# Optimization experiments

Measured on AMD Instinct MI355X. Metric: run time of the kernel, lower is better.

## Reference

```python
import jax, jax.numpy as jnp
import numpy as np

SEQ = 512; WIN = [4, 4, 4]; INNER = 5; DM = 256; H = 4; DK = 64; NEG = -1e9

def _all_sizes():
    s = [SEQ]
    for w in WIN:
        s.append(s[-1] // w)
    return s

def _build_mask():
    # Pyraformer get_mask: intra-scale band (inner_size) + inter-scale parent/child links.
    sizes = _all_sizes(); N = sum(sizes)
    starts = np.cumsum([0] + sizes)
    allow = np.zeros((N, N), bool)
    iw = INNER // 2
    for li, sz in enumerate(sizes):
        st = int(starts[li])
        for i in range(st, st + sz):
            allow[i, max(i - iw, st):min(i + iw + 1, st + sz)] = True
    for li in range(1, len(sizes)):
        st = int(starts[li])
        for i in range(st, st + sizes[li]):
            ls = int(starts[li - 1]) + (i - st) * WIN[li - 1]
            rs = st if i == st + sizes[li] - 1 else int(starts[li - 1]) + (i - st + 1) * WIN[li - 1]
            allow[i, ls:rs] = True
            allow[ls:rs, i] = True
    return jnp.asarray(~allow)  # True = blocked

def _build_indexes():
    # Pyraformer refer_points: for each base position, index of its node at every scale.
    sizes = _all_sizes(); starts = np.cumsum([0] + sizes)
    idx = np.zeros((SEQ, len(sizes)), np.int32)
    for i in range(SEQ):
        cur = i
        idx[i, 0] = cur
        for j in range(1, len(sizes)):
            inner = cur - int(starts[j - 1])
            cur = int(starts[j]) + min(inner // WIN[j - 1], sizes[j] - 1)
            idx[i, j] = cur
    return jnp.asarray(idx)

def _pos_enc(L, D):
    pos = np.arange(L)[:, None]
    div = np.exp(np.arange(0, D, 2) * (-np.log(10000.0) / D))
    pe = np.zeros((L, D), np.float32)
    pe[:, 0::2] = np.sin(pos * div)
    pe[:, 1::2] = np.cos(pos * div)
    return jnp.asarray(pe)

MASK = _build_mask()
INDEXES = _build_indexes()
PE = _pos_enc(SEQ, DM)
DN = ('NCH', 'OIH', 'NCH')

def _ln(x, g, b, eps=1e-5):
    m = x.mean(-1, keepdims=True)
    v = ((x - m) ** 2).mean(-1, keepdims=True)
    return (x - m) * jax.lax.rsqrt(v + eps) * g + b

def _forward(x_enc, x_mark, W_val, W_time, b_time, W_down, b_down, W_conv, b_conv, bn_g, bn_b, W_up, b_up, ln_c_g, ln_c_b, Wq, bq, Wk, bk, Wv, bv, Wo, bo, ln1_g, ln1_b, W1f, b1f, W2f, b2f, ln2_g, ln2_b, Wp, bp):
    B = x_enc.shape[0]
    # DataEmbedding: circular k=3 token conv + time-feature linear + fixed positional
    xt = jnp.pad(x_enc.transpose(0, 2, 1), ((0, 0), (0, 0), (1, 1)), mode='wrap')
    val = jax.lax.conv_general_dilated(xt, W_val, (1,), 'VALID', dimension_numbers=DN).transpose(0, 2, 1)
    emb = val + x_mark @ W_time + b_time + PE[None]  # [B, SEQ, DM]
    # CSCM Bottleneck_Construct: down-proj, strided conv pooling per scale, up-proj, concat, LN
    t = (emb @ W_down + b_down).transpose(0, 2, 1)  # [B, 64, SEQ]
    pooled = []
    for i in range(len(WIN)):
        t = jax.lax.conv_general_dilated(t, W_conv[i], (WIN[i],), 'VALID', dimension_numbers=DN) + b_conv[i][None, :, None]
        t = jax.nn.elu(t * bn_g[i][None, :, None] + bn_b[i][None, :, None])
        pooled.append(t)
    pooled = jnp.concatenate(pooled, axis=2).transpose(0, 2, 1) @ W_up + b_up  # [B, 168, DM]
    x = _ln(jnp.concatenate([emb, pooled], axis=1), ln_c_g, ln_c_b)  # [B, 680, DM]
    N = x.shape[1]
    scale = np.float32(1.0 / np.sqrt(DK))
    for l in range(Wq.shape[0]):
        q = (x @ Wq[l] + bq[l]).reshape(B, N, H, DK).transpose(0, 2, 1, 3)
        k = (x @ Wk[l] + bk[l]).reshape(B, N, H, DK).transpose(0, 2, 1, 3)
        v = (x @ Wv[l] + bv[l]).reshape(B, N, H, DK).transpose(0, 2, 1, 3)
        s = jnp.einsum('bhqd,bhkd->bhqk', q, k) * scale
        s = jnp.where(MASK[None, None], NEG, s)
        o = jnp.einsum('bhqk,bhkd->bhqd', jax.nn.softmax(s, axis=-1), v)
        o = o.transpose(0, 2, 1, 3).reshape(B, N, DM) @ Wo[l] + bo[l]
        x = _ln(x + o, ln1_g[l], ln1_b[l])  # post-norm (normalize_before=False)
        f = jax.nn.relu(x @ W1f[l] + b1f[l]) @ W2f[l] + b2f[l]
        x = _ln(x + f, ln2_g[l], ln2_b[l])
    # FC decoder path: gather each position's multi-scale nodes, concat features
    gathered = x[:, INDEXES.reshape(-1)].reshape(B, SEQ, -1)  # [B, SEQ, 4*DM]
    return gathered[:, -1] @ Wp + bp  # [B, 96]

def setup_inputs() -> dict:
    key = jax.random.key(0)
    ks = iter(jax.random.split(key, 64))
    def w(shape, s=0.05):
        return jax.random.normal(next(ks), shape, jnp.float32) * s
    d = {}
    d['x_enc'] = jax.random.normal(next(ks), (32, SEQ, 1), jnp.float32)
    d['x_mark'] = jax.random.normal(next(ks), (32, SEQ, 4), jnp.float32)
    d['W_val'] = w((DM, 1, 3))
    d['W_time'] = w((4, DM)); d['b_time'] = jnp.zeros((DM,), jnp.float32)
    d['W_down'] = w((DM, 64)); d['b_down'] = jnp.zeros((64,), jnp.float32)
    d['W_conv'] = w((3, 64, 64, 4)); d['b_conv'] = jnp.zeros((3, 64), jnp.float32)
    d['bn_g'] = jnp.ones((3, 64), jnp.float32); d['bn_b'] = jnp.zeros((3, 64), jnp.float32)
    d['W_up'] = w((64, DM)); d['b_up'] = jnp.zeros((DM,), jnp.float32)
    d['ln_c_g'] = jnp.ones((DM,), jnp.float32); d['ln_c_b'] = jnp.zeros((DM,), jnp.float32)
    d['Wq'] = w((2, DM, DM)); d['bq'] = jnp.zeros((2, DM), jnp.float32)
    d['Wk'] = w((2, DM, DM)); d['bk'] = jnp.zeros((2, DM), jnp.float32)
    d['Wv'] = w((2, DM, DM)); d['bv'] = jnp.zeros((2, DM), jnp.float32)
    d['Wo'] = w((2, DM, DM)); d['bo'] = jnp.zeros((2, DM), jnp.float32)
    d['ln1_g'] = jnp.ones((2, DM), jnp.float32); d['ln1_b'] = jnp.zeros((2, DM), jnp.float32)
    d['W1f'] = w((2, DM, 512)); d['b1f'] = jnp.zeros((2, 512), jnp.float32)
    d['W2f'] = w((2, 512, DM)); d['b2f'] = jnp.zeros((2, DM), jnp.float32)
    d['ln2_g'] = jnp.ones((2, DM), jnp.float32); d['ln2_b'] = jnp.zeros((2, DM), jnp.float32)
    d['Wp'] = w((4 * DM, 96)); d['bp'] = jnp.zeros((96,), jnp.float32)
    return d

def reference(x_enc, x_mark, W_val, W_time, b_time, W_down, b_down, W_conv, b_conv, bn_g, bn_b, W_up, b_up, ln_c_g, ln_c_b, Wq, bq, Wk, bk, Wv, bv, Wo, bo, ln1_g, ln1_b, W1f, b1f, W2f, b2f, ln2_g, ln2_b, Wp, bp):
    return _forward(x_enc, x_mark, W_val, W_time, b_time, W_down, b_down, W_conv, b_conv, bn_g, bn_b, W_up, b_up, ln_c_g, ln_c_b, Wq, bq, Wk, bk, Wv, bv, Wo, bo, ln1_g, ln1_b, W1f, b1f, W2f, b2f, ln2_g, ln2_b, Wp, bp)
```

## Files before the change

### kernel.cpp

```cpp
#include <hip/hip_runtime.h>
#include <hip/hip_bf16.h>
#include <math.h>

#define B 32
#define SEQ 512
#define NTOK 680
#define DM 256
#define FF 512
#define NROWS (B*NTOK)

using bf16x8 = __attribute__((ext_vector_type(8))) short;
using f32x4  = __attribute__((ext_vector_type(4))) float;
using u32x4  = __attribute__((ext_vector_type(4))) unsigned int;
typedef __hip_bfloat16 bf16;

__device__ __forceinline__ unsigned short f2bf(float f) {
    union { float f; unsigned u; } x; x.f = f;
    unsigned r = (x.u + 0x7fffu + ((x.u >> 16) & 1u)) >> 16;
    return (unsigned short)r;
}
__device__ __forceinline__ float bfu2f(unsigned short u) {
    union { unsigned u; float f; } x; x.u = ((unsigned)u) << 16;
    return x.f;
}
__device__ __forceinline__ void dotu(unsigned a, unsigned b, float& s) {
    union { unsigned u; float f; } al, ah, bl, bh;
    al.u = a << 16; ah.u = a & 0xffff0000u;
    bl.u = b << 16; bh.u = b & 0xffff0000u;
    s = fmaf(al.f, bl.f, s);
    s = fmaf(ah.f, bh.f, s);
}

__global__ __launch_bounds__(256) void emb_kernel(
    const float* __restrict__ x_enc, const float* __restrict__ x_mark,
    const float* __restrict__ W_val, const float* __restrict__ W_time,
    const float* __restrict__ b_time, float* __restrict__ X, bf16* __restrict__ Xe)
{
    int bs = blockIdx.x;
    int b = bs >> 9, s = bs & 511;
    int d = threadIdx.x;
    int sm1 = (s + 511) & 511, sp1 = (s + 1) & 511;
    float x0 = x_enc[b*512 + sm1];
    float x1 = x_enc[b*512 + s];
    float x2 = x_enc[b*512 + sp1];
    float val = x0 * W_val[d*3+0] + x1 * W_val[d*3+1] + x2 * W_val[d*3+2];
    const float* mk = &x_mark[(size_t)bs*4];
    float tm = mk[0]*W_time[d] + mk[1]*W_time[256+d] + mk[2]*W_time[512+d] + mk[3]*W_time[768+d];
    int i2 = d & ~1;
    float div = expf((float)i2 * (-9.210340371976184f / 256.0f));
    float ang = (float)s * div;
    float pe = (d & 1) ? cosf(ang) : sinf(ang);
    float out = val + tm + b_time[d] + pe;
    X[((size_t)(b*NTOK + s))*DM + d] = out;
    ((unsigned short*)Xe)[(size_t)bs*DM + d] = f2bf(out);
}

__global__ __launch_bounds__(64) void conv_kernel(
    const float* __restrict__ in, int inRPB, int inOff,
    float* __restrict__ Pool, int outOff, int Lout,
    const float* __restrict__ W_conv, const float* __restrict__ b_conv,
    const float* __restrict__ bn_g, const float* __restrict__ bn_b, int sc)
{
    __shared__ float lds[256];
    int blk = blockIdx.x;
    int b = blk / Lout, p = blk % Lout;
    int t = threadIdx.x;
    for (int u = t; u < 256; u += 64)
        lds[u] = in[((size_t)(b*inRPB + inOff + p*4 + (u >> 6)))*64 + (u & 63)];
    __syncthreads();
    float acc = b_conv[sc*64 + t];
    const float* w = &W_conv[(size_t)(sc*64 + t)*256];
    #pragma unroll 4
    for (int ci = 0; ci < 64; ++ci) {
        #pragma unroll
        for (int tap = 0; tap < 4; ++tap)
            acc = fmaf(lds[tap*64 + ci], w[ci*4 + tap], acc);
    }
    float v = acc * bn_g[sc*64 + t] + bn_b[sc*64 + t];
    v = v > 0.f ? v : expm1f(v);
    Pool[((size_t)(b*168 + outOff + p))*64 + t] = v;
}

__global__ __launch_bounds__(256) void up_kernel(
    const float* __restrict__ Pool, const float* __restrict__ W_up,
    const float* __restrict__ b_up, float* __restrict__ X)
{
    __shared__ float row[64];
    int blk = blockIdx.x;
    int b = blk / 168, p = blk % 168;
    int d = threadIdx.x;
    if (d < 64) row[d] = Pool[(size_t)blk*64 + d];
    __syncthreads();
    float acc = b_up[d];
    #pragma unroll 8
    for (int k = 0; k < 64; ++k) acc = fmaf(row[k], W_up[k*256 + d], acc);
    X[((size_t)(b*NTOK + 512 + p))*DM + d] = acc;
}

__global__ __launch_bounds__(256) void ln_kernel(
    const float* __restrict__ Xf, bf16* __restrict__ Xio,
    const float* __restrict__ g, const float* __restrict__ bta)
{
    int r = blockIdx.x*4 + (threadIdx.x >> 6);
    int lane = threadIdx.x & 63;
    float4 v = ((const float4*)(Xf + (size_t)r*DM))[lane];
    float s = v.x + v.y + v.z + v.w;
    #pragma unroll
    for (int o = 32; o; o >>= 1) s += __shfl_xor(s, o);
    float mean = s * (1.0f/256.0f);
    float dx = v.x-mean, dy = v.y-mean, dz = v.z-mean, dw = v.w-mean;
    float q = dx*dx + dy*dy + dz*dz + dw*dw;
    #pragma unroll
    for (int o = 32; o; o >>= 1) q += __shfl_xor(q, o);
    float inv = rsqrtf(q*(1.0f/256.0f) + 1e-5f);
    float4 gg = ((const float4*)g)[lane];
    float4 bb = ((const float4*)bta)[lane];
    float ox = dx*inv*gg.x + bb.x;
    float oy = dy*inv*gg.y + bb.y;
    float oz = dz*inv*gg.z + bb.z;
    float ow = dw*inv*gg.w + bb.w;
    unsigned u0 = (unsigned)f2bf(ox) | ((unsigned)f2bf(oy) << 16);
    unsigned u1 = (unsigned)f2bf(oz) | ((unsigned)f2bf(ow) << 16);
    ((uint2*)(Xio + (size_t)r*DM))[lane] = make_uint2(u0, u1);
}

__global__ void nbr_kernel(int* __restrict__ nbr, int* __restrict__ ncnt)
{
    int i = blockIdx.x * 64 + threadIdx.x;
    if (i >= NTOK) return;
    const int starts[5] = {0, 512, 640, 672, 680};
    int si = (i < 512) ? 0 : (i < 640) ? 1 : (i < 672) ? 2 : 3;
    int st = starts[si], en = starts[si+1];
    int idx = i - st;
    int cnt = 0;
    if (si >= 1) {
        int cs = starts[si-1] + idx*4;
        #pragma unroll
        for (int c = 0; c < 4; ++c) nbr[i*16 + cnt++] = cs + c;
    }
    int lo = (i-2 > st) ? i-2 : st;
    int hi = (i+2 < en-1) ? i+2 : en-1;
    for (int j = lo; j <= hi; ++j) nbr[i*16 + cnt++] = j;
    if (si <= 2) nbr[i*16 + cnt++] = starts[si+1] + (idx >> 2);
    ncnt[i] = cnt;
}

__global__ __launch_bounds__(256) void attn_kernel(
    const bf16* __restrict__ Q, const bf16* __restrict__ K,
    const bf16* __restrict__ V, bf16* __restrict__ O,
    const int* __restrict__ nbr, const int* __restrict__ ncnt)
{
    __shared__ float wsm[4][16];
    __shared__ int   jsm[4][16];
    int flat = blockIdx.x;
    int row = (flat & 7) * (NROWS/8) + (flat >> 3);
    int n = row % NTOK, b = row / NTOK;
    int h = threadIdx.x >> 6;
    int lane = threadIdx.x & 63;
    int j = lane >> 2, g = lane & 3;
    int cnt = ncnt[n];
    int nj = (j < cnt) ? nbr[n*16 + j] : n;
    int jr = b*NTOK + nj;

    const uint4* qp = (const uint4*)(Q + (size_t)row*DM + h*64 + g*16);
    const uint4* kp = (const uint4*)(K + (size_t)jr*DM + h*64 + g*16);
    uint4 qa = qp[0], qb = qp[1];
    uint4 ka = kp[0], kb = kp[1];
    float s = 0.f;
    dotu(qa.x, ka.x, s); dotu(qa.y, ka.y, s); dotu(qa.z, ka.z, s); dotu(qa.w, ka.w, s);
    dotu(qb.x, kb.x, s); dotu(qb.y, kb.y, s); dotu(qb.z, kb.z, s); dotu(qb.w, kb.w, s);
    s += __shfl_xor(s, 1);
    s += __shfl_xor(s, 2);
    s *= 0.125f;
    if (j >= cnt) s = -1e30f;
    float m = s;
    #pragma unroll
    for (int o = 4; o < 64; o <<= 1) m = fmaxf(m, __shfl_xor(m, o));
    float w = (j < cnt) ? expf(s - m) : 0.f;
    float den = w;
    #pragma unroll
    for (int o = 4; o < 64; o <<= 1) den += __shfl_xor(den, o);
    if (g == 0) { wsm[h][j] = w / den; jsm[h][j] = jr; }
    __syncthreads();

    float acc = 0.f;
    const unsigned short* Vu = (const unsigned short*)V;
    for (int jj = 0; jj < cnt; ++jj) {
        float wv = wsm[h][jj];
        int rr = jsm[h][jj];
        acc = fmaf(wv, bfu2f(Vu[(size_t)rr*DM + h*64 + lane]), acc);
    }
    ((unsigned short*)O)[(size_t)row*DM + h*64 + lane] = f2bf(acc);
}

struct WDesc { const float* src; bf16* dst; int K; int N; };
struct WTable { WDesc d[13]; };
__global__ __launch_bounds__(256) void wconv_kernel(WTable tbl)
{
    __shared__ float lds[32][33];
    WDesc ds = tbl.d[blockIdx.y];
    int ntn = ds.N >> 5;
    int ntiles = (ds.K >> 5) * ntn;
    int tile = blockIdx.x;
    if (tile >= ntiles) return;
    int k0 = (tile / ntn) * 32, n0 = (tile % ntn) * 32;
    int t = threadIdx.x;
    int r = t >> 3, c4 = (t & 7) * 4;
    float4 v = *(const float4*)(ds.src + (size_t)(k0 + r)*ds.N + n0 + c4);
    lds[r][c4+0] = v.x; lds[r][c4+1] = v.y; lds[r][c4+2] = v.z; lds[r][c4+3] = v.w;
    __syncthreads();
    unsigned u0 = (unsigned)f2bf(lds[c4+0][r]) | ((unsigned)f2bf(lds[c4+1][r]) << 16);
    unsigned u1 = (unsigned)f2bf(lds[c4+2][r]) | ((unsigned)f2bf(lds[c4+3][r]) << 16);
    *(uint2*)((unsigned short*)ds.dst + (size_t)(n0 + r)*ds.K + k0 + c4) = make_uint2(u0, u1);
}

__global__ __launch_bounds__(256) void wpt_kernel(
    const float* __restrict__ Wp, float* __restrict__ WpT)
{
    int e = blockIdx.x*256 + threadIdx.x;
    int o = e % 96, k = e / 96;
    WpT[(size_t)o*1024 + k] = Wp[(size_t)k*96 + o];
}

__global__ __launch_bounds__(512) void qkv_kernel(
    const bf16* __restrict__ Xh,
    const bf16* __restrict__ WqT, const bf16* __restrict__ WkT, const bf16* __restrict__ WvT,
    const float* __restrict__ bq, const float* __restrict__ bk, const float* __restrict__ bv,
    bf16* __restrict__ Qh, bf16* __restrict__ Kh, bf16* __restrict__ Vh)
{
    __shared__ __align__(16) char smem[16384 + 16896];
    uint4* AsU = (uint4*)smem;
    const bf16x8* Asv = (const bf16x8*)smem;
    unsigned short* ctb = (unsigned short*)(smem + 16384);

    int t = threadIdx.x;
    int lane = t & 63, w = t >> 6;
    int nwg = gridDim.x;
    int wg = (blockIdx.x & 7) * (nwg >> 3) + (blockIdx.x >> 3);
    int row0 = wg * 32;
    const unsigned short* Xu = (const unsigned short*)Xh;

    #pragma unroll
    for (int i = 0; i < 2; ++i) {
        int gg = t + i*512, r = gg >> 5, c = gg & 31;
        AsU[r*32 + (c ^ (r & 7))] = *(const uint4*)(Xu + (size_t)(row0 + r)*DM + c*8);
    }
    __syncthreads();

    #pragma unroll
    for (int z = 0; z < 3; ++z) {
        const unsigned short* Wu = (const unsigned short*)((z == 0) ? WqT : (z == 1) ? WkT : WvT);
        const float* bias = (z == 0) ? bq : (z == 1) ? bk : bv;
        bf16* Op = (z == 0) ? Qh : (z == 1) ? Kh : Vh;

        f32x4 acc[2][2];
        #pragma unroll
        for (int m = 0; m < 2; ++m)
            #pragma unroll
            for (int nn = 0; nn < 2; ++nn)
                #pragma unroll
                for (int q = 0; q < 4; ++q) acc[m][nn][q] = 0.f;
        float bv_[2];
        #pragma unroll
        for (int nn = 0; nn < 2; ++nn) bv_[nn] = bias[w*32 + nn*16 + (lane & 15)];

        #pragma unroll
        for (int kt = 0; kt < 256; kt += 32) {
            int cg = (kt >> 3) + (lane >> 4);
            bf16x8 af[2];
            #pragma unroll
            for (int m = 0; m < 2; ++m) {
                int ar = m*16 + (lane & 15);
                af[m] = Asv[ar*32 + (cg ^ (ar & 7))];
            }
            #pragma unroll
            for (int nn = 0; nn < 2; ++nn) {
                int nrow = w*32 + nn*16 + (lane & 15);
                bf16x8 bfr = *(const bf16x8*)(Wu + (size_t)nrow*256 + kt + (lane >> 4)*8);
                #pragma unroll
                for (int m = 0; m < 2; ++m)
                    acc[m][nn] = __builtin_amdgcn_mfma_f32_16x16x32_bf16(af[m], bfr, acc[m][nn], 0, 0, 0);
            }
        }

        __syncthreads();
        #pragma unroll
        for (int m = 0; m < 2; ++m)
            #pragma unroll
            for (int nn = 0; nn < 2; ++nn) {
                int col = w*32 + nn*16 + (lane & 15);
                #pragma unroll
                for (int q = 0; q < 4; ++q) {
                    int row = m*16 + (lane >> 4)*4 + q;
                    ctb[row*264 + col] = f2bf(acc[m][nn][q] + bv_[nn]);
                }
            }
        __syncthreads();
        #pragma unroll
        for (int i = 0; i < 2; ++i) {
            int idx = t + i*512;
            int row = idx >> 5, c16 = idx & 31;
            u32x4 uv = *(const u32x4*)(ctb + row*264 + c16*8);
            *(u32x4*)((unsigned short*)Op + (size_t)(row0 + row)*DM + c16*8) = uv;
        }
    }
}

#define CSTR 260
__global__ __launch_bounds__(512) void wo_ln_kernel(
    const bf16* __restrict__ Ob, bf16* __restrict__ Xh,
    const bf16* __restrict__ WoT, const float* __restrict__ bo,
    const float* __restrict__ g, const float* __restrict__ bta)
{
    __shared__ __align__(16) char smem[16384 + 33280];
    uint4* AsU = (uint4*)smem;
    const bf16x8* Asv = (const bf16x8*)smem;
    float* ctile = (float*)(smem + 16384);

    int t = threadIdx.x;
    int lane = t & 63, w = t >> 6;
    int nwg = gridDim.x;
    int wg = (blockIdx.x & 7) * (nwg >> 3) + (blockIdx.x >> 3);
    int row0 = wg * 32;
    const unsigned short* Obu = (const unsigned short*)Ob;
    const unsigned short* Xu  = (const unsigned short*)Xh;
    const unsigned short* Wu  = (const unsigned short*)WoT;

    #pragma unroll
    for (int i = 0; i < 2; ++i) {
        int gg = t + i*512, r = gg >> 5, c = gg & 31;
        AsU[r*32 + (c ^ (r & 7))] = *(const uint4*)(Obu + (size_t)(row0 + r)*DM + c*8);
    }

    f32x4 acc[2][2];
    #pragma unroll
    for (int m = 0; m < 2; ++m)
        #pragma unroll
        for (int nn = 0; nn < 2; ++nn)
            #pragma unroll
            for (int q = 0; q < 4; ++q) acc[m][nn][q] = 0.f;
    float bv[2];
    #pragma unroll
    for (int nn = 0; nn < 2; ++nn) bv[nn] = bo[w*32 + nn*16 + (lane & 15)];
    __syncthreads();

    #pragma unroll
    for (int kt = 0; kt < 256; kt += 32) {
        int cg = (kt >> 3) + (lane >> 4);
        bf16x8 af[2];
        #pragma unroll
        for (int m = 0; m < 2; ++m) {
            int ar = m*16 + (lane & 15);
            af[m] = Asv[ar*32 + (cg ^ (ar & 7))];
        }
        #pragma unroll
        for (int nn = 0; nn < 2; ++nn) {
            int nrow = w*32 + nn*16 + (lane & 15);
            bf16x8 bfr = *(const bf16x8*)(Wu + (size_t)nrow*256 + kt + (lane >> 4)*8);
            #pragma unroll
            for (int m = 0; m < 2; ++m)
                acc[m][nn] = __builtin_amdgcn_mfma_f32_16x16x32_bf16(af[m], bfr, acc[m][nn], 0, 0, 0);
        }
    }

    __syncthreads();
    #pragma unroll
    for (int m = 0; m < 2; ++m)
        #pragma unroll
        for (int nn = 0; nn < 2; ++nn) {
            int col = w*32 + nn*16 + (lane & 15);
            #pragma unroll
            for (int q = 0; q < 4; ++q) {
                int row = m*16 + (lane >> 4)*4 + q;
                ctile[row*CSTR + col] = acc[m][nn][q] + bv[nn];
            }
        }
    __syncthreads();
    #pragma unroll
    for (int rr = 0; rr < 4; ++rr) {
        int row = w*4 + rr;
        float4 v = *(const float4*)(ctile + row*CSTR + lane*4);
        uint2 xu = *(const uint2*)(Xu + (size_t)(row0 + row)*DM + lane*4);
        v.x += bfu2f((unsigned short)(xu.x & 0xffffu));
        v.y += bfu2f((unsigned short)(xu.x >> 16));
        v.z += bfu2f((unsigned short)(xu.y & 0xffffu));
        v.w += bfu2f((unsigned short)(xu.y >> 16));
        float s = v.x + v.y + v.z + v.w;
        #pragma unroll
        for (int o = 32; o; o >>= 1) s += __shfl_xor(s, o);
        float mean = s * (1.0f/256.0f);
        float dx = v.x-mean, dy = v.y-mean, dz = v.z-mean, dw = v.w-mean;
        float q2 = dx*dx + dy*dy + dz*dz + dw*dw;
        #pragma unroll
        for (int o = 32; o; o >>= 1) q2 += __shfl_xor(q2, o);
        float inv = rsqrtf(q2*(1.0f/256.0f) + 1e-5f);
        float4 gg = ((const float4*)g)[lane];
        float4 bb = ((const float4*)bta)[lane];
        float ox = dx*inv*gg.x + bb.x;
        float oy = dy*inv*gg.y + bb.y;
        float oz = dz*inv*gg.z + bb.z;
        float ow = dw*inv*gg.w + bb.w;
        unsigned u0 = (unsigned)f2bf(ox) | ((unsigned)f2bf(oy) << 16);
        unsigned u1 = (unsigned)f2bf(oz) | ((unsigned)f2bf(ow) << 16);
        *(uint2*)((unsigned short*)Xh + (size_t)(row0 + row)*DM + lane*4) = make_uint2(u0, u1);
    }
}

#define HSTR 280
__global__ __launch_bounds__(512) void ff_kernel(
    bf16* __restrict__ Xh,
    const bf16* __restrict__ W1t, const float* __restrict__ b1,
    const bf16* __restrict__ W2t, const float* __restrict__ b2,
    const float* __restrict__ g, const float* __restrict__ bta)
{
    __shared__ __align__(16) char smem[16384 + 33280];
    uint4* AsU = (uint4*)smem;
    const bf16x8* Asv = (const bf16x8*)smem;
    unsigned short* hT = (unsigned short*)(smem + 16384);
    float* ctile = (float*)(smem + 16384);

    int t = threadIdx.x;
    int lane = t & 63, w = t >> 6;
    int nwg = gridDim.x;
    int wg = (blockIdx.x & 7) * (nwg >> 3) + (blockIdx.x >> 3);
    int row0 = wg * 32;
    const unsigned short* Xu = (const unsigned short*)Xh;

    #pragma unroll
    for (int i = 0; i < 2; ++i) {
        int gg = t + i*512, r = gg >> 5, c = gg & 31;
        AsU[r*32 + (c ^ (r & 7))] = *(const uint4*)(Xu + (size_t)(row0 + r)*DM + c*8);
    }

    f32x4 acc2[2][2];
    #pragma unroll
    for (int m = 0; m < 2; ++m)
        #pragma unroll
        for (int nn = 0; nn < 2; ++nn)
            #pragma unroll
            for (int q = 0; q < 4; ++q) acc2[m][nn][q] = 0.f;
    float b2v[2];
    #pragma unroll
    for (int nn = 0; nn < 2; ++nn) b2v[nn] = b2[w*32 + nn*16 + (lane & 15)];
    __syncthreads();

    const unsigned short* W1u = (const unsigned short*)W1t;
    const unsigned short* W2u = (const unsigned short*)W2t;

    #pragma unroll
    for (int half = 0; half < 2; ++half) {
        f32x4 acc1[2][2];
        #pragma unroll
        for (int m = 0; m < 2; ++m)
            #pragma unroll
            for (int nn = 0; nn < 2; ++nn)
                #pragma unroll
                for (int q = 0; q < 4; ++q) acc1[m][nn][q] = 0.f;
        #pragma unroll
        for (int kt = 0; kt < 256; kt += 32) {
            int cg = (kt >> 3) + (lane >> 4);
            bf16x8 af[2];
            #pragma unroll
            for (int m = 0; m < 2; ++m) {
                int ar = m*16 + (lane & 15);
                af[m] = Asv[ar*32 + (cg ^ (ar & 7))];
            }
            #pragma unroll
            for (int nn = 0; nn < 2; ++nn) {
                int nrow = half*256 + w*32 + nn*16 + (lane & 15);
                bf16x8 bfr = *(const bf16x8*)(W1u + (size_t)nrow*256 + kt + (lane >> 4)*8);
                #pragma unroll
                for (int m = 0; m < 2; ++m)
                    acc1[m][nn] = __builtin_amdgcn_mfma_f32_16x16x32_bf16(af[m], bfr, acc1[m][nn], 0, 0, 0);
            }
        }
        float b1v[2];
        #pragma unroll
        for (int nn = 0; nn < 2; ++nn) b1v[nn] = b1[half*256 + w*32 + nn*16 + (lane & 15)];
        __syncthreads();
        #pragma unroll
        for (int m = 0; m < 2; ++m)
            #pragma unroll
            for (int nn = 0; nn < 2; ++nn) {
                int col = w*32 + nn*16 + (lane & 15);
                #pragma unroll
                for (int q = 0; q < 4; ++q) {
                    int row = m*16 + (lane >> 4)*4 + q;
                    hT[row*HSTR + col] = f2bf(fmaxf(acc1[m][nn][q] + b1v[nn], 0.f));
                }
            }
        __syncthreads();
        #pragma unroll
        for (int kt = 0; kt < 256; kt += 32) {
            bf16x8 af[2];
            #pragma unroll
            for (int m = 0; m < 2; ++m) {
                int ar = m*16 + (lane & 15);
                af[m] = *(const bf16x8*)(hT + ar*HSTR + kt + (lane >> 4)*8);
            }
            #pragma unroll
            for (int nn = 0; nn < 2; ++nn) {
                int nrow = w*32 + nn*16 + (lane & 15);
                bf16x8 bfr = *(const bf16x8*)(W2u + (size_t)nrow*512 + half*256 + kt + (lane >> 4)*8);
                #pragma unroll
                for (int m = 0; m < 2; ++m)
                    acc2[m][nn] = __builtin_amdgcn_mfma_f32_16x16x32_bf16(af[m], bfr, acc2[m][nn], 0, 0, 0);
            }
        }
    }
    __syncthreads();
    #pragma unroll
    for (int m = 0; m < 2; ++m)
        #pragma unroll
        for (int nn = 0; nn < 2; ++nn) {
            int col = w*32 + nn*16 + (lane & 15);
            #pragma unroll
            for (int q = 0; q < 4; ++q) {
                int row = m*16 + (lane >> 4)*4 + q;
                ctile[row*CSTR + col] = acc2[m][nn][q] + b2v[nn];
            }
        }
    __syncthreads();
    #pragma unroll
    for (int rr = 0; rr < 4; ++rr) {
        int row = w*4 + rr;
        float4 v = *(const float4*)(ctile + row*CSTR + lane*4);
        uint2 xu = *(const uint2*)(Xu + (size_t)(row0 + row)*DM + lane*4);
        v.x += bfu2f((unsigned short)(xu.x & 0xffffu));
        v.y += bfu2f((unsigned short)(xu.x >> 16));
        v.z += bfu2f((unsigned short)(xu.y & 0xffffu));
        v.w += bfu2f((unsigned short)(xu.y >> 16));
        float s = v.x + v.y + v.z + v.w;
        #pragma unroll
        for (int o = 32; o; o >>= 1) s += __shfl_xor(s, o);
        float mean = s * (1.0f/256.0f);
        float dx = v.x-mean, dy = v.y-mean, dz = v.z-mean, dw = v.w-mean;
        float q2 = dx*dx + dy*dy + dz*dz + dw*dw;
        #pragma unroll
        for (int o = 32; o; o >>= 1) q2 += __shfl_xor(q2, o);
        float inv = rsqrtf(q2*(1.0f/256.0f) + 1e-5f);
        float4 gg = ((const float4*)g)[lane];
        float4 bb = ((const float4*)bta)[lane];
        float ox = dx*inv*gg.x + bb.x;
        float oy = dy*inv*gg.y + bb.y;
        float oz = dz*inv*gg.z + bb.z;
        float ow = dw*inv*gg.w + bb.w;
        unsigned u0 = (unsigned)f2bf(ox) | ((unsigned)f2bf(oy) << 16);
        unsigned u1 = (unsigned)f2bf(oz) | ((unsigned)f2bf(ow) << 16);
        *(uint2*)((unsigned short*)Xh + (size_t)(row0 + row)*DM + lane*4) = make_uint2(u0, u1);
    }
}

__global__ __launch_bounds__(256) void mfma_gemm_dn(
    const bf16* __restrict__ A, const bf16* __restrict__ Wt,
    const float* __restrict__ bias, float* __restrict__ Op)
{
    __shared__ __align__(16) char smem[34816];
    uint4* AsU = (uint4*)smem;
    uint4* BsU = (uint4*)(smem + 16384);
    const bf16x8* Asv = (const bf16x8*)smem;
    const bf16x8* Bsv = (const bf16x8*)(smem + 16384);
    const int KD = 256, Nc = 64;

    int t = threadIdx.x;
    int lane = t & 63, wid = t >> 6;
    int wm = wid >> 1, wn = wid & 1;
    int nwg = gridDim.x;
    int wg = (blockIdx.x & 7) * (nwg >> 3) + (blockIdx.x >> 3);
    int row0 = wg * 128;
    int n0 = 0;

    f32x4 acc[4][2];
    #pragma unroll
    for (int i = 0; i < 4; ++i)
        #pragma unroll
        for (int jn = 0; jn < 2; ++jn)
            #pragma unroll
            for (int r = 0; r < 4; ++r) acc[i][jn][r] = 0.f;

    uint4 pa[4], pb[2];
    #pragma unroll
    for (int i = 0; i < 4; ++i) {
        int gg = t + i*256, r = gg >> 3, c = gg & 7;
        pa[i] = *reinterpret_cast<const uint4*>(A + (size_t)(row0 + r)*KD + c*8);
    }
    #pragma unroll
    for (int i = 0; i < 2; ++i) {
        int gg = t + i*256, r = gg >> 3, c = gg & 7;
        pb[i] = *reinterpret_cast<const uint4*>(Wt + (size_t)(n0 + r)*KD + c*8);
    }

    #pragma unroll
    for (int kt = 0; kt < KD; kt += 64) {
        __syncthreads();
        #pragma unroll
        for (int i = 0; i < 4; ++i) {
            int gg = t + i*256, r = gg >> 3, c = gg & 7;
            AsU[r*8 + (c ^ (r & 7))] = pa[i];
        }
        #pragma unroll
        for (int i = 0; i < 2; ++i) {
            int gg = t + i*256, r = gg >> 3, c = gg & 7;
            BsU[r*8 + (c ^ (r & 7))] = pb[i];
        }
        __syncthreads();
        if (kt + 64 < KD) {
            #pragma unroll
            for (int i = 0; i < 4; ++i) {
                int gg = t + i*256, r = gg >> 3, c = gg & 7;
                pa[i] = *reinterpret_cast<const uint4*>(A + (size_t)(row0 + r)*KD + (kt + 64) + c*8);
            }
            #pragma unroll
            for (int i = 0; i < 2; ++i) {
                int gg = t + i*256, r = gg >> 3, c = gg & 7;
                pb[i] = *reinterpret_cast<const uint4*>(Wt + (size_t)(n0 + r)*KD + (kt + 64) + c*8);
            }
        }
        #pragma unroll
        for (int ks = 0; ks < 2; ++ks) {
            int cg = ks*4 + (lane >> 4);
            bf16x8 af[4], bfr[2];
            #pragma unroll
            for (int m = 0; m < 4; ++m) {
                int ar = wm*64 + m*16 + (lane & 15);
                af[m] = Asv[ar*8 + (cg ^ (ar & 7))];
            }
            #pragma unroll
            for (int nn = 0; nn < 2; ++nn) {
                int br = wn*32 + nn*16 + (lane & 15);
                bfr[nn] = Bsv[br*8 + (cg ^ (br & 7))];
            }
            #pragma unroll
            for (int m = 0; m < 4; ++m)
                #pragma unroll
                for (int nn = 0; nn < 2; ++nn)
                    acc[m][nn] = __builtin_amdgcn_mfma_f32_16x16x32_bf16(af[m], bfr[nn], acc[m][nn], 0, 0, 0);
        }
    }

    __syncthreads();
    float* ctile = (float*)smem;
    #pragma unroll
    for (int m = 0; m < 4; ++m) {
        #pragma unroll
        for (int nn = 0; nn < 2; ++nn) {
            int cc = wn*32 + nn*16 + (lane & 15);
            float bcol = bias[n0 + cc];
            #pragma unroll
            for (int r = 0; r < 4; ++r) {
                int rr = wm*64 + m*16 + (lane >> 4)*4 + r;
                ctile[rr*68 + cc] = acc[m][nn][r] + bcol;
            }
        }
    }
    __syncthreads();
    int c4 = (t & 15) * 4;
    #pragma unroll
    for (int rr = t >> 4; rr < 128; rr += 16) {
        float4 v = *reinterpret_cast<const float4*>(ctile + rr*68 + c4);
        *reinterpret_cast<float4*>(Op + (size_t)(row0 + rr)*Nc + n0 + c4) = v;
    }
}

__global__ __launch_bounds__(512) void final_kernel(
    const bf16* __restrict__ Xh, const float* __restrict__ WpT,
    const float* __restrict__ bp, float* __restrict__ out)
{
    __shared__ float rows[1024];
    int b = blockIdx.x, t = threadIdx.x;
    int lane = t & 63, w = t >> 6;
    const unsigned short* Xu = (const unsigned short*)Xh;
    for (int u = t; u < 1024; u += 512) {
        int g = u >> 8;
        int id = (g == 0) ? 511 : (g == 1) ? 639 : (g == 2) ? 671 : 679;
        rows[u] = bfu2f(Xu[((size_t)(b*NTOK + id))*DM + (u & 255)]);
    }
    __syncthreads();
    #pragma unroll
    for (int oi = 0; oi < 12; ++oi) {
        int o = w*12 + oi;
        float acc = 0.f;
        #pragma unroll
        for (int i = 0; i < 16; ++i) {
            int k = i*64 + lane;
            acc = fmaf(rows[k], WpT[(size_t)o*1024 + k], acc);
        }
        #pragma unroll
        for (int off = 32; off; off >>= 1) acc += __shfl_xor(acc, off);
        if (lane == 0) out[b*96 + o] = acc + bp[o];
    }
}

extern "C" void kernel_launch(void* const* d_in, const int* in_sizes, int n_in,
                              void* d_out, int out_size, void* d_ws, size_t ws_size,
                              hipStream_t stream)
{
    const float* x_enc  = (const float*)d_in[0];
    const float* x_mark = (const float*)d_in[1];
    const float* W_val  = (const float*)d_in[2];
    const float* W_time = (const float*)d_in[3];
    const float* b_time = (const float*)d_in[4];
    const float* W_down = (const float*)d_in[5];
    const float* b_down = (const float*)d_in[6];
    const float* W_conv = (const float*)d_in[7];
    const float* b_conv = (const float*)d_in[8];
    const float* bn_g   = (const float*)d_in[9];
    const float* bn_b   = (const float*)d_in[10];
    const float* W_up   = (const float*)d_in[11];
    const float* b_up   = (const float*)d_in[12];
    const float* ln_c_g = (const float*)d_in[13];
    const float* ln_c_b = (const float*)d_in[14];
    const float* Wq     = (const float*)d_in[15];
    const float* bq     = (const float*)d_in[16];
    const float* Wk     = (const float*)d_in[17];
    const float* bk     = (const float*)d_in[18];
    const float* Wv     = (const float*)d_in[19];
    const float* bv     = (const float*)d_in[20];
    const float* Wo     = (const float*)d_in[21];
    const float* bo     = (const float*)d_in[22];
    const float* ln1_g  = (const float*)d_in[23];
    const float* ln1_b  = (const float*)d_in[24];
    const float* W1f    = (const float*)d_in[25];
    const float* b1f    = (const float*)d_in[26];
    const float* W2f    = (const float*)d_in[27];
    const float* b2f    = (const float*)d_in[28];
    const float* ln2_g  = (const float*)d_in[29];
    const float* ln2_b  = (const float*)d_in[30];
    const float* Wp     = (const float*)d_in[31];
    const float* bp     = (const float*)d_in[32];

    const size_t RB = (size_t)NROWS * DM;
    float* ws = (float*)d_ws;
    float* X    = ws;
    float* Td   = X + RB;
    float* Pool = Td + (size_t)B*SEQ*64;
    float* WpT  = Pool + (size_t)B*168*64;
    bf16* bws   = (bf16*)(WpT + 96*1024);
    bf16* Xh   = bws;
    bf16* Qh   = Xh  + RB;
    bf16* Kh   = Qh  + RB;
    bf16* Vh   = Kh  + RB;
    bf16* Obh  = Vh  + RB;
    bf16* Xe   = Obh + RB;
    bf16* WqT  = Xe  + (size_t)B*SEQ*DM;
    bf16* WkT  = WqT + 2*65536;
    bf16* WvT  = WkT + 2*65536;
    bf16* WoT  = WvT + 2*65536;
    bf16* W1T  = WoT + 2*65536;
    bf16* W2T  = W1T + 2*131072;
    bf16* WdT  = W2T + 2*131072;
    int*  nbr  = (int*)(WdT + 64*256);
    int*  ncnt = nbr + NTOK*16;

    WTable tbl;
    for (int l = 0; l < 2; ++l) {
        tbl.d[l*6+0] = { Wq  + (size_t)l*65536,  WqT + (size_t)l*65536,  256, 256 };
        tbl.d[l*6+1] = { Wk  + (size_t)l*65536,  WkT + (size_t)l*65536,  256, 256 };
        tbl.d[l*6+2] = { Wv  + (size_t)l*65536,  WvT + (size_t)l*65536,  256, 256 };
        tbl.d[l*6+3] = { Wo  + (size_t)l*65536,  WoT + (size_t)l*65536,  256, 256 };
        tbl.d[l*6+4] = { W1f + (size_t)l*131072, W1T + (size_t)l*131072, 256, 512 };
        tbl.d[l*6+5] = { W2f + (size_t)l*131072, W2T + (size_t)l*131072, 512, 256 };
    }
    tbl.d[12] = { W_down, WdT, 256, 64 };
    wconv_kernel<<<dim3(128, 13), 256, 0, stream>>>(tbl);
    wpt_kernel<<<384, 256, 0, stream>>>(Wp, WpT);

    emb_kernel<<<B*SEQ, 256, 0, stream>>>(x_enc, x_mark, W_val, W_time, b_time, X, Xe);
    mfma_gemm_dn<<<128, 256, 0, stream>>>(Xe, WdT, b_down, Td);
    conv_kernel<<<B*128, 64, 0, stream>>>(Td, 512, 0,   Pool, 0,   128, W_conv, b_conv, bn_g, bn_b, 0);
    conv_kernel<<<B*32,  64, 0, stream>>>(Pool, 168, 0,  Pool, 128, 32,  W_conv, b_conv, bn_g, bn_b, 1);
    conv_kernel<<<B*8,   64, 0, stream>>>(Pool, 168, 128,Pool, 160, 8,   W_conv, b_conv, bn_g, bn_b, 2);
    up_kernel<<<B*168, 256, 0, stream>>>(Pool, W_up, b_up, X);
    ln_kernel<<<NROWS/4, 256, 0, stream>>>(X, Xh, ln_c_g, ln_c_b);
    nbr_kernel<<<11, 64, 0, stream>>>(nbr, ncnt);

    for (int l = 0; l < 2; ++l) {
        const bf16* wqt = WqT + (size_t)l*65536;
        const bf16* wkt = WkT + (size_t)l*65536;
        const bf16* wvt = WvT + (size_t)l*65536;
        const bf16* wot = WoT + (size_t)l*65536;
        const bf16* w1t = W1T + (size_t)l*131072;
        const bf16* w2t = W2T + (size_t)l*131072;
        const float* bq_ = bq + l*DM; const float* bk_ = bk + l*DM;
        const float* bv_ = bv + l*DM; const float* bo_ = bo + l*DM;
        const float* b1_ = b1f + l*FF; const float* b2_ = b2f + l*DM;

        qkv_kernel<<<680, 512, 0, stream>>>(Xh, wqt, wkt, wvt, bq_, bk_, bv_, Qh, Kh, Vh);
        attn_kernel<<<NROWS, 256, 0, stream>>>(Qh, Kh, Vh, Obh, nbr, ncnt);
        wo_ln_kernel<<<680, 512, 0, stream>>>(Obh, Xh, wot, bo_, ln1_g + l*DM, ln1_b + l*DM);
        ff_kernel<<<680, 512, 0, stream>>>(Xh, w1t, b1_, w2t, b2_, ln2_g + l*DM, ln2_b + l*DM);
    }

    final_kernel<<<B, 512, 0, stream>>>(Xh, WpT, bp, (float*)d_out);
}
```

Before: 398.3 us.

## Fuse Wo+LN1 with FFN+LN2 into one kernel and batch weight prefetch

Merges the output-projection/LayerNorm kernel and the feed-forward/LayerNorm kernel into a single launch. The LN1 result stays in shared memory as the FFN input and residual, so it is no longer written to and re-read from global memory. It also restructures the MFMA K-loops in the QKV, Wo and FFN GEMMs to load eight weight fragments into registers per half-K before issuing the MFMAs, which gives more memory-level parallelism. The prefetch raises register pressure and the fused kernel is longer, which may reduce occupancy.

```diff
diff --git a/kernel.cpp b/kernel.cpp
--- a/kernel.cpp
+++ b/kernel.cpp
@@ -265,21 +265,29 @@
         for (int nn = 0; nn < 2; ++nn) bv_[nn] = bias[w*32 + nn*16 + (lane & 15)];
 
         #pragma unroll
-        for (int kt = 0; kt < 256; kt += 32) {
-            int cg = (kt >> 3) + (lane >> 4);
-            bf16x8 af[2];
-            #pragma unroll
-            for (int m = 0; m < 2; ++m) {
-                int ar = m*16 + (lane & 15);
-                af[m] = Asv[ar*32 + (cg ^ (ar & 7))];
-            }
-            #pragma unroll
-            for (int nn = 0; nn < 2; ++nn) {
+        for (int kh = 0; kh < 2; ++kh) {
+            bf16x8 pw[8];
+            #pragma unroll
+            for (int i = 0; i < 8; ++i) {
+                int kt = kh*128 + (i >> 1)*32, nn = i & 1;
                 int nrow = w*32 + nn*16 + (lane & 15);
-                bf16x8 bfr = *(const bf16x8*)(Wu + (size_t)nrow*256 + kt + (lane >> 4)*8);
-                #pragma unroll
-                for (int m = 0; m < 2; ++m)
-                    acc[m][nn] = __builtin_amdgcn_mfma_f32_16x16x32_bf16(af[m], bfr, acc[m][nn], 0, 0, 0);
+                pw[i] = *(const bf16x8*)(Wu + (size_t)nrow*256 + kt + (lane >> 4)*8);
+            }
+            #pragma unroll
+            for (int ki = 0; ki < 4; ++ki) {
+                int kt = kh*128 + ki*32;
+                int cg = (kt >> 3) + (lane >> 4);
+                bf16x8 af[2];
+                #pragma unroll
+                for (int m = 0; m < 2; ++m) {
+                    int ar = m*16 + (lane & 15);
+                    af[m] = Asv[ar*32 + (cg ^ (ar & 7))];
+                }
+                #pragma unroll
+                for (int nn = 0; nn < 2; ++nn)
+                    #pragma unroll
+                    for (int m = 0; m < 2; ++m)
+                        acc[m][nn] = __builtin_amdgcn_mfma_f32_16x16x32_bf16(af[m], pw[ki*2+nn], acc[m][nn], 0, 0, 0);
             }
         }
 
@@ -307,15 +315,21 @@
 }
 
 #define CSTR 260
-__global__ __launch_bounds__(512) void wo_ln_kernel(
+#define HSTR 280
+__global__ __launch_bounds__(512) void layer2_kernel(
     const bf16* __restrict__ Ob, bf16* __restrict__ Xh,
     const bf16* __restrict__ WoT, const float* __restrict__ bo,
-    const float* __restrict__ g, const float* __restrict__ bta)
+    const float* __restrict__ g1, const float* __restrict__ b1n,
+    const bf16* __restrict__ W1t, const float* __restrict__ b1,
+    const bf16* __restrict__ W2t, const float* __restrict__ b2,
+    const float* __restrict__ g2, const float* __restrict__ b2n)
 {
     __shared__ __align__(16) char smem[16384 + 33280];
     uint4* AsU = (uint4*)smem;
     const bf16x8* Asv = (const bf16x8*)smem;
+    unsigned short* Asu16 = (unsigned short*)smem;
     float* ctile = (float*)(smem + 16384);
+    unsigned short* hT = (unsigned short*)(smem + 16384);
 
     int t = threadIdx.x;
     int lane = t & 63, w = t >> 6;
@@ -324,58 +338,70 @@
     int row0 = wg * 32;
     const unsigned short* Obu = (const unsigned short*)Ob;
     const unsigned short* Xu  = (const unsigned short*)Xh;
-    const unsigned short* Wu  = (const unsigned short*)WoT;
+    const unsigned short* WoU = (const unsigned short*)WoT;
+    const unsigned short* W1u = (const unsigned short*)W1t;
+    const unsigned short* W2u = (const unsigned short*)W2t;
 
     #pragma unroll
     for (int i = 0; i < 2; ++i) {
         int gg = t + i*512, r = gg >> 5, c = gg & 31;
         AsU[r*32 + (c ^ (r & 7))] = *(const uint4*)(Obu + (size_t)(row0 + r)*DM + c*8);
     }
-
-    f32x4 acc[2][2];
-    #pragma unroll
-    for (int m = 0; m < 2; ++m)
-        #pragma unroll
-        for (int nn = 0; nn < 2; ++nn)
-            #pragma unroll
-            for (int q = 0; q < 4; ++q) acc[m][nn][q] = 0.f;
-    float bv[2];
-    #pragma unroll
-    for (int nn = 0; nn < 2; ++nn) bv[nn] = bo[w*32 + nn*16 + (lane & 15)];
-    __syncthreads();
-
-    #pragma unroll
-    for (int kt = 0; kt < 256; kt += 32) {
-        int cg = (kt >> 3) + (lane >> 4);
-        bf16x8 af[2];
-        #pragma unroll
-        for (int m = 0; m < 2; ++m) {
-            int ar = m*16 + (lane & 15);
-            af[m] = Asv[ar*32 + (cg ^ (ar & 7))];
-        }
-        #pragma unroll
-        for (int nn = 0; nn < 2; ++nn) {
-            int nrow = w*32 + nn*16 + (lane & 15);
-            bf16x8 bfr = *(const bf16x8*)(Wu + (size_t)nrow*256 + kt + (lane >> 4)*8);
-            #pragma unroll
-            for (int m = 0; m < 2; ++m)
-                acc[m][nn] = __builtin_amdgcn_mfma_f32_16x16x32_bf16(af[m], bfr, acc[m][nn], 0, 0, 0);
-        }
-    }
-
-    __syncthreads();
-    #pragma unroll
-    for (int m = 0; m < 2; ++m)
-        #pragma unroll
-        for (int nn = 0; nn < 2; ++nn) {
-            int col = w*32 + nn*16 + (lane & 15);
-            #pragma unroll
-            for (int q = 0; q < 4; ++q) {
-                int row = m*16 + (lane >> 4)*4 + q;
-                ctile[row*CSTR + col] = acc[m][nn][q] + bv[nn];
-            }
-        }
-    __syncthreads();
+    __syncthreads();
+
+    {
+        f32x4 acc[2][2];
+        #pragma unroll
+        for (int m = 0; m < 2; ++m)
+            #pragma unroll
+            for (int nn = 0; nn < 2; ++nn)
+                #pragma unroll
+                for (int q = 0; q < 4; ++q) acc[m][nn][q] = 0.f;
+        float bvv[2];
+        #pragma unroll
+        for (int nn = 0; nn < 2; ++nn) bvv[nn] = bo[w*32 + nn*16 + (lane & 15)];
+
+        #pragma unroll
+        for (int kh = 0; kh < 2; ++kh) {
+            bf16x8 pw[8];
+            #pragma unroll
+            for (int i = 0; i < 8; ++i) {
+                int kt = kh*128 + (i >> 1)*32, nn = i & 1;
+                int nrow = w*32 + nn*16 + (lane & 15);
+                pw[i] = *(const bf16x8*)(WoU + (size_t)nrow*256 + kt + (lane >> 4)*8);
+            }
+            #pragma unroll
+            for (int ki = 0; ki < 4; ++ki) {
+                int kt = kh*128 + ki*32;
+                int cg = (kt >> 3) + (lane >> 4);
+                bf16x8 af[2];
+                #pragma unroll
+                for (int m = 0; m < 2; ++m) {
+                    int ar = m*16 + (lane & 15);
+                    af[m] = Asv[ar*32 + (cg ^ (ar & 7))];
+                }
+                #pragma unroll
+                for (int nn = 0; nn < 2; ++nn)
+                    #pragma unroll
+                    for (int m = 0; m < 2; ++m)
+                        acc[m][nn] = __builtin_amdgcn_mfma_f32_16x16x32_bf16(af[m], pw[ki*2+nn], acc[m][nn], 0, 0, 0);
+            }
+        }
+
+        #pragma unroll
+        for (int m = 0; m < 2; ++m)
+            #pragma unroll
+            for (int nn = 0; nn < 2; ++nn) {
+                int col = w*32 + nn*16 + (lane & 15);
+                #pragma unroll
+                for (int q = 0; q < 4; ++q) {
+                    int row = m*16 + (lane >> 4)*4 + q;
+                    ctile[row*CSTR + col] = acc[m][nn][q] + bvv[nn];
+                }
+            }
+    }
+    __syncthreads();
+
     #pragma unroll
     for (int rr = 0; rr < 4; ++rr) {
         int row = w*4 + rr;
@@ -394,43 +420,17 @@
         #pragma unroll
         for (int o = 32; o; o >>= 1) q2 += __shfl_xor(q2, o);
         float inv = rsqrtf(q2*(1.0f/256.0f) + 1e-5f);
-        float4 gg = ((const float4*)g)[lane];
-        float4 bb = ((const float4*)bta)[lane];
+        float4 gg = ((const float4*)g1)[lane];
+        float4 bb = ((const float4*)b1n)[lane];
         float ox = dx*inv*gg.x + bb.x;
         float oy = dy*inv*gg.y + bb.y;
         float oz = dz*inv*gg.z + bb.z;
         float ow = dw*inv*gg.w + bb.w;
         unsigned u0 = (unsigned)f2bf(ox) | ((unsigned)f2bf(oy) << 16);
         unsigned u1 = (unsigned)f2bf(oz) | ((unsigned)f2bf(ow) << 16);
-        *(uint2*)((unsigned short*)Xh + (size_t)(row0 + row)*DM + lane*4) = make_uint2(u0, u1);
-    }
-}
-
-#define HSTR 280
-__global__ __launch_bounds__(512) void ff_kernel(
-    bf16* __restrict__ Xh,
-    const bf16* __restrict__ W1t, const float* __restrict__ b1,
-    const bf16* __restrict__ W2t, const float* __restrict__ b2,
-    const float* __restrict__ g, const float* __restrict__ bta)
-{
-    __shared__ __align__(16) char smem[16384 + 33280];
-    uint4* AsU = (uint4*)smem;
-    const bf16x8* Asv = (const bf16x8*)smem;
-    unsigned short* hT = (unsigned short*)(smem + 16384);
-    float* ctile = (float*)(smem + 16384);
-
-    int t = threadIdx.x;
-    int lane = t & 63, w = t >> 6;
-    int nwg = gridDim.x;
-    int wg = (blockIdx.x & 7) * (nwg >> 3) + (blockIdx.x >> 3);
-    int row0 = wg * 32;
-    const unsigned short* Xu = (const unsigned short*)Xh;
-
-    #pragma unroll
-    for (int i = 0; i < 2; ++i) {
-        int gg = t + i*512, r = gg >> 5, c = gg & 31;
-        AsU[r*32 + (c ^ (r & 7))] = *(const uint4*)(Xu + (size_t)(row0 + r)*DM + c*8);
-    }
+        *(uint2*)(Asu16 + row*256 + (((lane>>1) ^ (row & 7))*8) + (lane & 1)*4) = make_uint2(u0, u1);
+    }
+    __syncthreads();
 
     f32x4 acc2[2][2];
     #pragma unroll
@@ -442,10 +442,6 @@
     float b2v[2];
     #pragma unroll
     for (int nn = 0; nn < 2; ++nn) b2v[nn] = b2[w*32 + nn*16 + (lane & 15)];
-    __syncthreads();
-
-    const unsigned short* W1u = (const unsigned short*)W1t;
-    const unsigned short* W2u = (const unsigned short*)W2t;
 
     #pragma unroll
     for (int half = 0; half < 2; ++half) {
@@ -457,21 +453,29 @@
                 #pragma unroll
                 for (int q = 0; q < 4; ++q) acc1[m][nn][q] = 0.f;
         #pragma unroll
-        for (int kt = 0; kt < 256; kt += 32) {
-            int cg = (kt >> 3) + (lane >> 4);
-            bf16x8 af[2];
-            #pragma unroll
-            for (int m = 0; m < 2; ++m) {
-                int ar = m*16 + (lane & 15);
-                af[m] = Asv[ar*32 + (cg ^ (ar & 7))];
-            }
-            #pragma unroll
-            for (int nn = 0; nn < 2; ++nn) {
+        for (int kh = 0; kh < 2; ++kh) {
+            bf16x8 pw[8];
+            #pragma unroll
+            for (int i = 0; i < 8; ++i) {
+                int kt = kh*128 + (i >> 1)*32, nn = i & 1;
                 int nrow = half*256 + w*32 + nn*16 + (lane & 15);
-                bf16x8 bfr = *(const bf16x8*)(W1u + (size_t)nrow*256 + kt + (lane >> 4)*8);
-                #pragma unroll
-                for (int m = 0; m < 2; ++m)
-                    acc1[m][nn] = __builtin_amdgcn_mfma_f32_16x16x32_bf16(af[m], bfr, acc1[m][nn], 0, 0, 0);
+                pw[i] = *(const bf16x8*)(W1u + (size_t)nrow*256 + kt + (lane >> 4)*8);
+            }
+            #pragma unroll
+            for (int ki = 0; ki < 4; ++ki) {
+                int kt = kh*128 + ki*32;
+                int cg = (kt >> 3) + (lane >> 4);
+                bf16x8 af[2];
+                #pragma unroll
+                for (int m = 0; m < 2; ++m) {
+                    int ar = m*16 + (lane & 15);
+                    af[m] = Asv[ar*32 + (cg ^ (ar & 7))];
+                }
+                #pragma unroll
+                for (int nn = 0; nn < 2; ++nn)
+                    #pragma unroll
+                    for (int m = 0; m < 2; ++m)
+                        acc1[m][nn] = __builtin_amdgcn_mfma_f32_16x16x32_bf16(af[m], pw[ki*2+nn], acc1[m][nn], 0, 0, 0);
             }
         }
         float b1v[2];
@@ -491,24 +495,33 @@
             }
         __syncthreads();
         #pragma unroll
-        for (int kt = 0; kt < 256; kt += 32) {
-            bf16x8 af[2];
-            #pragma unroll
-            for (int m = 0; m < 2; ++m) {
-                int ar = m*16 + (lane & 15);
-                af[m] = *(const bf16x8*)(hT + ar*HSTR + kt + (lane >> 4)*8);
-            }
-            #pragma unroll
-            for (int nn = 0; nn < 2; ++nn) {
+        for (int kh = 0; kh < 2; ++kh) {
+            bf16x8 pw[8];
+            #pragma unroll
+            for (int i = 0; i < 8; ++i) {
+                int kt = kh*128 + (i >> 1)*32, nn = i & 1;
                 int nrow = w*32 + nn*16 + (lane & 15);
-                bf16x8 bfr = *(const bf16x8*)(W2u + (size_t)nrow*512 + half*256 + kt + (lane >> 4)*8);
-                #pragma unroll
-                for (int m = 0; m < 2; ++m)
-                    acc2[m][nn] = __builtin_amdgcn_mfma_f32_16x16x32_bf16(af[m], bfr, acc2[m][nn], 0, 0, 0);
-            }
-        }
-    }
-    __syncthreads();
+                pw[i] = *(const bf16x8*)(W2u + (size_t)nrow*512 + half*256 + kt + (lane >> 4)*8);
+            }
+            #pragma unroll
+            for (int ki = 0; ki < 4; ++ki) {
+                int kt = kh*128 + ki*32;
+                bf16x8 af[2];
+                #pragma unroll
+                for (int m = 0; m < 2; ++m) {
+                    int ar = m*16 + (lane & 15);
+                    af[m] = *(const bf16x8*)(hT + ar*HSTR + kt + (lane >> 4)*8);
+                }
+                #pragma unroll
+                for (int nn = 0; nn < 2; ++nn)
+                    #pragma unroll
+                    for (int m = 0; m < 2; ++m)
+                        acc2[m][nn] = __builtin_amdgcn_mfma_f32_16x16x32_bf16(af[m], pw[ki*2+nn], acc2[m][nn], 0, 0, 0);
+            }
+        }
+        __syncthreads();
+    }
+
     #pragma unroll
     for (int m = 0; m < 2; ++m)
         #pragma unroll
@@ -525,7 +538,7 @@
     for (int rr = 0; rr < 4; ++rr) {
         int row = w*4 + rr;
         float4 v = *(const float4*)(ctile + row*CSTR + lane*4);
-        uint2 xu = *(const uint2*)(Xu + (size_t)(row0 + row)*DM + lane*4);
+        uint2 xu = *(const uint2*)(Asu16 + row*256 + (((lane>>1) ^ (row & 7))*8) + (lane & 1)*4);
         v.x += bfu2f((unsigned short)(xu.x & 0xffffu));
         v.y += bfu2f((unsigned short)(xu.x >> 16));
         v.z += bfu2f((unsigned short)(xu.y & 0xffffu));
@@ -539,8 +552,8 @@
         #pragma unroll
         for (int o = 32; o; o >>= 1) q2 += __shfl_xor(q2, o);
         float inv = rsqrtf(q2*(1.0f/256.0f) + 1e-5f);
-        float4 gg = ((const float4*)g)[lane];
-        float4 bb = ((const float4*)bta)[lane];
+        float4 gg = ((const float4*)g2)[lane];
+        float4 bb = ((const float4*)b2n)[lane];
         float ox = dx*inv*gg.x + bb.x;
         float oy = dy*inv*gg.y + bb.y;
         float oz = dz*inv*gg.z + bb.z;
@@ -787,8 +800,8 @@
 
         qkv_kernel<<<680, 512, 0, stream>>>(Xh, wqt, wkt, wvt, bq_, bk_, bv_, Qh, Kh, Vh);
         attn_kernel<<<NROWS, 256, 0, stream>>>(Qh, Kh, Vh, Obh, nbr, ncnt);
-        wo_ln_kernel<<<680, 512, 0, stream>>>(Obh, Xh, wot, bo_, ln1_g + l*DM, ln1_b + l*DM);
-        ff_kernel<<<680, 512, 0, stream>>>(Xh, w1t, b1_, w2t, b2_, ln2_g + l*DM, ln2_b + l*DM);
+        layer2_kernel<<<680, 512, 0, stream>>>(Obh, Xh, wot, bo_,
+            ln1_g + l*DM, ln1_b + l*DM, w1t, b1_, w2t, b2_, ln2_g + l*DM, ln2_b + l*DM);
     }
 
     final_kernel<<<B, 512, 0, stream>>>(Xh, WpT, bp, (float*)d_out);
```

After: 391.0 us. No clear change (-1.8%).
